# Performance work log

Hardware: AMD Instinct MI355X
Metric: run time of the kernel (lower is better)

Reference implementation:

```python
import jax, jax.numpy as jnp
import numpy as np

D = 16          # u_emb_size
LAYER_NUM = 2   # CAN layer_num

def setup_inputs() -> dict:
    key = jax.random.key(0)
    k1, k2 = jax.random.split(key)
    B, N = 16384, 50
    user_emb = jax.random.normal(k1, (B, N, D), dtype=jnp.float32)
    # item side packs per-sample MLP params: [W0(d*d), b0(d), W1(d*d), b1(d)]
    item_emb = jax.random.normal(k2, (B, D * (D + 1) * LAYER_NUM), dtype=jnp.float32)
    return {"user_emb": user_emb, "item_emb": item_emb}

def reference(user_emb, item_emb):
    B = user_emb.shape[0]
    x = user_emb  # (B, N, D)
    off = 0
    for _ in range(LAYER_NUM):
        W = item_emb[:, off:off + D * D].reshape(B, D, D); off += D * D
        b = item_emb[:, off:off + D].reshape(B, 1, D);      off += D
        # per-sample batched matmul + bias + relu
        x = jax.nn.relu(jnp.einsum('bnd,bde->bne', x, W) + b)
    return x  # (B, N, D); is_seq=False, is_stacked=True -> return as-is
```

## Files before the change

### kernel.cpp

```cpp
#include <hip/hip_runtime.h>


#define CAN_D 16
#define CAN_N 50
#define CAN_PSTRIDE 544
#define WAVES_PER_BLOCK 4
#define YSTRIDE 20

typedef __attribute__((ext_vector_type(8))) short short8;
typedef __attribute__((ext_vector_type(4))) float f32x4;

union ABFrag { int i[4]; short8 v; };

__device__ __forceinline__ int pack2_bf16(float lo, float hi) {
    unsigned a = __builtin_bit_cast(unsigned, lo);
    unsigned b = __builtin_bit_cast(unsigned, hi);
    a = (a + 0x7FFFu + ((a >> 16) & 1u)) >> 16;
    b = (b + 0x7FFFu + ((b >> 16) & 1u)) & 0xFFFF0000u;
    return (int)(a | b);
}

__global__ __launch_bounds__(256) void can_kernel(
    const float* __restrict__ user_emb,
    const float* __restrict__ item_emb,
    float* __restrict__ out, int B)
{
    __shared__ __align__(16) float ybuf[WAVES_PER_BLOCK][4][16 * YSTRIDE];

    const int wave = threadIdx.x >> 6;
    const int lane = threadIdx.x & 63;
    const int s = blockIdx.x * WAVES_PER_BLOCK + wave;
    if (s >= B) return;

    const int n    = lane & 15;
    const int quad = lane >> 4;

    const float* __restrict__ P = item_emb + (size_t)s * CAN_PSTRIDE;

    ABFrag w0, w1;
    if (quad < 2) {
        const float* W0 = P + quad * 8 * CAN_D + n;
        const float* W1 = P + 272 + quad * 8 * CAN_D + n;
        float t0[8], t1[8];
#pragma unroll
        for (int j = 0; j < 8; ++j) { t0[j] = W0[j * CAN_D]; t1[j] = W1[j * CAN_D]; }
#pragma unroll
        for (int j = 0; j < 4; ++j) {
            w0.i[j] = pack2_bf16(t0[2 * j], t0[2 * j + 1]);
            w1.i[j] = pack2_bf16(t1[2 * j], t1[2 * j + 1]);
        }
    } else {
#pragma unroll
        for (int j = 0; j < 4; ++j) { w0.i[j] = 0; w1.i[j] = 0; }
    }
    const float b0 = P[256 + n];
    const float b1 = P[528 + n];

    const float* __restrict__ xbase = user_emb + (size_t)s * (CAN_N * CAN_D);

#pragma unroll
    for (int t = 0; t < 4; ++t) {
        ABFrag a0;
        if (quad < 2) {
            int row = t * 16 + n;
            if (row > CAN_N - 1) row = CAN_N - 1;
            const float4* px = (const float4*)(xbase + row * CAN_D + quad * 8);
            float4 u0 = px[0], u1 = px[1];
            a0.i[0] = pack2_bf16(u0.x, u0.y);
            a0.i[1] = pack2_bf16(u0.z, u0.w);
            a0.i[2] = pack2_bf16(u1.x, u1.y);
            a0.i[3] = pack2_bf16(u1.z, u1.w);
        } else {
#pragma unroll
            for (int j = 0; j < 4; ++j) a0.i[j] = 0;
        }

        f32x4 c0 = {b0, b0, b0, b0};
        c0 = __builtin_amdgcn_mfma_f32_16x16x32_bf16(a0.v, w0.v, c0, 0, 0, 0);

        float* yb = &ybuf[wave][t][0];
#pragma unroll
        for (int r = 0; r < 4; ++r)
            yb[(quad * 4 + r) * YSTRIDE + n] = fmaxf(c0[r], 0.0f);

        ABFrag a1;
        if (quad < 2) {
            const float* pr = yb + n * YSTRIDE + quad * 8;
            float4 v0 = *(const float4*)pr;
            float4 v1 = *(const float4*)(pr + 4);
            a1.i[0] = pack2_bf16(v0.x, v0.y);
            a1.i[1] = pack2_bf16(v0.z, v0.w);
            a1.i[2] = pack2_bf16(v1.x, v1.y);
            a1.i[3] = pack2_bf16(v1.z, v1.w);
        } else {
#pragma unroll
            for (int j = 0; j < 4; ++j) a1.i[j] = 0;
        }

        f32x4 c1 = {b1, b1, b1, b1};
        c1 = __builtin_amdgcn_mfma_f32_16x16x32_bf16(a1.v, w1.v, c1, 0, 0, 0);

#pragma unroll
        for (int r = 0; r < 4; ++r) {
            int grow = t * 16 + quad * 4 + r;
            if (grow < CAN_N)
                out[((size_t)s * CAN_N + grow) * CAN_D + n] = fmaxf(c1[r], 0.0f);
        }
    }
}

extern "C" void kernel_launch(void* const* d_in, const int* in_sizes, int n_in,
                              void* d_out, int out_size, void* d_ws, size_t ws_size,
                              hipStream_t stream) {
    const float* user_emb = (const float*)d_in[0];
    const float* item_emb = (const float*)d_in[1];
    float* out = (float*)d_out;

    const int B = in_sizes[0] / (CAN_N * CAN_D);
    const int blocks = (B + WAVES_PER_BLOCK - 1) / WAVES_PER_BLOCK;
    can_kernel<<<blocks, 256, 0, stream>>>(user_emb, item_emb, out, B);
}
```

Measured before the change: 127.4 us.

## Hoist all global loads up front and stage outputs through LDS for float4 stores

Result: no change. 126.5 us (-0.7%).

```diff
diff --git a/kernel.cpp b/kernel.cpp
--- a/kernel.cpp
+++ b/kernel.cpp
@@ -12,20 +12,18 @@
 
 union ABFrag { int i[4]; short8 v; };
 
-__device__ __forceinline__ int pack2_bf16(float lo, float hi) {
-    unsigned a = __builtin_bit_cast(unsigned, lo);
-    unsigned b = __builtin_bit_cast(unsigned, hi);
-    a = (a + 0x7FFFu + ((a >> 16) & 1u)) >> 16;
-    b = (b + 0x7FFFu + ((b >> 16) & 1u)) & 0xFFFF0000u;
-    return (int)(a | b);
+__device__ __forceinline__ int pack2(float lo, float hi) {
+    unsigned short ua = __builtin_bit_cast(unsigned short, (__bf16)lo);
+    unsigned short ub = __builtin_bit_cast(unsigned short, (__bf16)hi);
+    return (int)((unsigned)ua | ((unsigned)ub << 16));
 }
 
-__global__ __launch_bounds__(256) void can_kernel(
+__global__ __launch_bounds__(256, 5) void can_kernel(
     const float* __restrict__ user_emb,
     const float* __restrict__ item_emb,
     float* __restrict__ out, int B)
 {
-    __shared__ __align__(16) float ybuf[WAVES_PER_BLOCK][4][16 * YSTRIDE];
+    __shared__ __align__(16) float ybuf[WAVES_PER_BLOCK][2][16 * YSTRIDE];
 
     const int wave = threadIdx.x >> 6;
     const int lane = threadIdx.x & 63;
@@ -35,50 +33,65 @@
     const int n    = lane & 15;
     const int quad = lane >> 4;
 
-    const float* __restrict__ P = item_emb + (size_t)s * CAN_PSTRIDE;
+    const float* __restrict__ P     = item_emb + (size_t)s * CAN_PSTRIDE;
+    const float* __restrict__ xbase = user_emb + (size_t)s * (CAN_N * CAN_D);
+    float* __restrict__ obase       = out      + (size_t)s * (CAN_N * CAN_D);
+
+    float t0[8], t1[8];
+    if (quad < 2) {
+        const float* W0 = P + quad * 8 * CAN_D + n;
+        const float* W1 = P + 272 + quad * 8 * CAN_D + n;
+#pragma unroll
+        for (int j = 0; j < 8; ++j) { t0[j] = W0[j * CAN_D]; t1[j] = W1[j * CAN_D]; }
+    }
+    const float b0v = P[256 + n];
+    const float b1v = P[528 + n];
+
+    float4 xu0[4], xu1[4];
+#pragma unroll
+    for (int t = 0; t < 4; ++t) {
+        if (quad < 2) {
+            int row = t * 16 + n;
+            if (row > CAN_N - 1) row = CAN_N - 1;
+            const float4* px = (const float4*)(xbase + row * CAN_D + quad * 8);
+            xu0[t] = px[0];
+            xu1[t] = px[1];
+        }
+    }
 
     ABFrag w0, w1;
     if (quad < 2) {
-        const float* W0 = P + quad * 8 * CAN_D + n;
-        const float* W1 = P + 272 + quad * 8 * CAN_D + n;
-        float t0[8], t1[8];
-#pragma unroll
-        for (int j = 0; j < 8; ++j) { t0[j] = W0[j * CAN_D]; t1[j] = W1[j * CAN_D]; }
 #pragma unroll
         for (int j = 0; j < 4; ++j) {
-            w0.i[j] = pack2_bf16(t0[2 * j], t0[2 * j + 1]);
-            w1.i[j] = pack2_bf16(t1[2 * j], t1[2 * j + 1]);
+            w0.i[j] = pack2(t0[2 * j], t0[2 * j + 1]);
+            w1.i[j] = pack2(t1[2 * j], t1[2 * j + 1]);
         }
     } else {
 #pragma unroll
         for (int j = 0; j < 4; ++j) { w0.i[j] = 0; w1.i[j] = 0; }
     }
-    const float b0 = P[256 + n];
-    const float b1 = P[528 + n];
 
-    const float* __restrict__ xbase = user_emb + (size_t)s * (CAN_N * CAN_D);
+    ABFrag a0[4];
+#pragma unroll
+    for (int t = 0; t < 4; ++t) {
+        if (quad < 2) {
+            a0[t].i[0] = pack2(xu0[t].x, xu0[t].y);
+            a0[t].i[1] = pack2(xu0[t].z, xu0[t].w);
+            a0[t].i[2] = pack2(xu1[t].x, xu1[t].y);
+            a0[t].i[3] = pack2(xu1[t].z, xu1[t].w);
+        } else {
+#pragma unroll
+            for (int j = 0; j < 4; ++j) a0[t].i[j] = 0;
+        }
+    }
 
 #pragma unroll
     for (int t = 0; t < 4; ++t) {
-        ABFrag a0;
-        if (quad < 2) {
-            int row = t * 16 + n;
-            if (row > CAN_N - 1) row = CAN_N - 1;
-            const float4* px = (const float4*)(xbase + row * CAN_D + quad * 8);
-            float4 u0 = px[0], u1 = px[1];
-            a0.i[0] = pack2_bf16(u0.x, u0.y);
-            a0.i[1] = pack2_bf16(u0.z, u0.w);
-            a0.i[2] = pack2_bf16(u1.x, u1.y);
-            a0.i[3] = pack2_bf16(u1.z, u1.w);
-        } else {
-#pragma unroll
-            for (int j = 0; j < 4; ++j) a0.i[j] = 0;
-        }
+        float* yb = &ybuf[wave][t & 1][0];
 
-        f32x4 c0 = {b0, b0, b0, b0};
-        c0 = __builtin_amdgcn_mfma_f32_16x16x32_bf16(a0.v, w0.v, c0, 0, 0, 0);
+        f32x4 c0 = {b0v, b0v, b0v, b0v};
+        c0 = __builtin_amdgcn_mfma_f32_16x16x32_bf16(a0[t].v, w0.v, c0, 0, 0, 0);
 
-        float* yb = &ybuf[wave][t][0];
 #pragma unroll
         for (int r = 0; r < 4; ++r)
             yb[(quad * 4 + r) * YSTRIDE + n] = fmaxf(c0[r], 0.0f);
@@ -88,24 +101,28 @@
             const float* pr = yb + n * YSTRIDE + quad * 8;
             float4 v0 = *(const float4*)pr;
             float4 v1 = *(const float4*)(pr + 4);
-            a1.i[0] = pack2_bf16(v0.x, v0.y);
-            a1.i[1] = pack2_bf16(v0.z, v0.w);
-            a1.i[2] = pack2_bf16(v1.x, v1.y);
-            a1.i[3] = pack2_bf16(v1.z, v1.w);
+            a1.i[0] = pack2(v0.x, v0.y);
+            a1.i[1] = pack2(v0.z, v0.w);
+            a1.i[2] = pack2(v1.x, v1.y);
+            a1.i[3] = pack2(v1.z, v1.w);
         } else {
 #pragma unroll
             for (int j = 0; j < 4; ++j) a1.i[j] = 0;
         }
 
-        f32x4 c1 = {b1, b1, b1, b1};
+        f32x4 c1 = {b1v, b1v, b1v, b1v};
         c1 = __builtin_amdgcn_mfma_f32_16x16x32_bf16(a1.v, w1.v, c1, 0, 0, 0);
 
 #pragma unroll
-        for (int r = 0; r < 4; ++r) {
-            int grow = t * 16 + quad * 4 + r;
-            if (grow < CAN_N)
-                out[((size_t)s * CAN_N + grow) * CAN_D + n] = fmaxf(c1[r], 0.0f);
-        }
+        for (int r = 0; r < 4; ++r)
+            yb[(quad * 4 + r) * YSTRIDE + n] = fmaxf(c1[r], 0.0f);
+
+        const int srow = lane >> 2;
+        const int scol = lane & 3;
+        float4 ov = *(const float4*)(yb + srow * YSTRIDE + scol * 4);
+        const int grow = t * 16 + srow;
+        if (grow < CAN_N)
+            *(float4*)(obase + grow * CAN_D + scol * 4) = ov;
     }
 }
 
```
